# Performance work log

Measured on AMD Instinct MI355X. Metric: run time of the kernel, lower is better.

The kernel has to match this reference:

```python
import jax, jax.numpy as jnp
import numpy as np

EPS = 1e-8
NHEAD = 4
N_ITER = 3


def _ln(x, g, b):
    mu = jnp.mean(x, axis=-1, keepdims=True)
    var = jnp.var(x, axis=-1, keepdims=True)
    return (x - mu) / jnp.sqrt(var + 1e-5) * g + b


def _forward(inputs, eps, init_mu, init_logvar, Wk, Wv, Wq,
             ln_in_g, ln_in_b, ln_slot_g, ln_slot_b, ln_res_g, ln_res_b,
             gru_Wih, gru_Whh, gru_bih, gru_bhh, mlp_W1, mlp_W2, mlp_b2):
    B, N, _ = inputs.shape
    D = init_mu.shape[-1]
    dh = D // NHEAD
    # reparameterized init of the figure representation  [B, D]
    rep = init_mu + jnp.exp(0.5 * init_logvar) * eps
    x = _ln(inputs, ln_in_g, ln_in_b)
    # [B, H, N, dh]; k is pre-scaled by sqrt(nhead) as in the source
    k = (x @ Wk).reshape(B, N, NHEAD, dh).transpose(0, 2, 1, 3) * (NHEAD ** 0.5)
    v = (x @ Wv).reshape(B, N, NHEAD, dh).transpose(0, 2, 1, 3)

    def step(rep):
        q = (_ln(rep, ln_slot_g, ln_slot_b) @ Wq).reshape(B, NHEAD, dh)
        # sigmoid attention, normalized over the patch dim N
        w = jax.nn.sigmoid(jnp.einsum('bhnd,bhd->bhn', k, q)) + EPS
        w = w / jnp.sum(w, axis=2, keepdims=True)          # [B, H, N]
        att = jnp.einsum('bhn,bhnd->bhd', w, v).reshape(B, D)
        # GRUCell(input=att, hidden=rep)
        gi = att @ gru_Wih.T + gru_bih
        gh = rep @ gru_Whh.T + gru_bhh
        ir, iz, ig = jnp.split(gi, 3, axis=-1)
        hr, hz, hg = jnp.split(gh, 3, axis=-1)
        r = jax.nn.sigmoid(ir + hr)
        z = jax.nn.sigmoid(iz + hz)
        g = jnp.tanh(ig + r * hg)
        new = (1.0 - z) * g + z * rep
        # residual MLP
        new = new + jax.nn.relu(_ln(new, ln_res_g, ln_res_b) @ mlp_W1) @ mlp_W2 + mlp_b2
        return new, w

    for _ in range(N_ITER):
        rep, w = step(rep)
    # approx_implicit_grad: one extra step from a detached latent
    rep, w = step(jax.lax.stop_gradient(rep))
    return rep, jnp.sum(w, axis=1)[..., None]   # ([B, D], [B, N, 1])


def setup_inputs() -> dict:
    key = jax.random.key(0)
    ks = jax.random.split(key, 12)
    B, N, Din, D, H = 128, 4096, 256, 256, 1024
    s = lambda f: 1.0 / np.sqrt(f)
    return {
        'inputs': jax.random.normal(ks[0], (B, N, Din), jnp.float32),
        'eps': jax.random.normal(ks[1], (B, D), jnp.float32),
        'init_mu': jax.random.normal(ks[2], (1, D), jnp.float32) * 0.02,
        'init_logvar': jax.random.normal(ks[3], (1, D), jnp.float32) * 0.02,
        'Wk': jax.random.normal(ks[4], (Din, D), jnp.float32) * s(Din),
        'Wv': jax.random.normal(ks[5], (Din, D), jnp.float32) * s(Din),
        'Wq': jax.random.normal(ks[6], (D, D), jnp.float32) * s(D),
        'ln_in_g': jnp.ones((Din,), jnp.float32),
        'ln_in_b': jnp.zeros((Din,), jnp.float32),
        'ln_slot_g': jnp.ones((D,), jnp.float32),
        'ln_slot_b': jnp.zeros((D,), jnp.float32),
        'ln_res_g': jnp.ones((D,), jnp.float32),
        'ln_res_b': jnp.zeros((D,), jnp.float32),
        'gru_Wih': jax.random.normal(ks[7], (3 * D, D), jnp.float32) * s(D),
        'gru_Whh': jax.random.normal(ks[8], (3 * D, D), jnp.float32) * s(D),
        'gru_bih': jnp.zeros((3 * D,), jnp.float32),
        'gru_bhh': jnp.zeros((3 * D,), jnp.float32),
        'mlp_W1': jax.random.normal(ks[9], (D, H), jnp.float32) * s(D),
        'mlp_W2': jax.random.normal(ks[10], (H, D), jnp.float32) * s(H),
        'mlp_b2': jnp.zeros((D,), jnp.float32),
    }


def reference(inputs, eps, init_mu, init_logvar, Wk, Wv, Wq,
              ln_in_g, ln_in_b, ln_slot_g, ln_slot_b, ln_res_g, ln_res_b,
              gru_Wih, gru_Whh, gru_bih, gru_bhh, mlp_W1, mlp_W2, mlp_b2):
    return _forward(inputs, eps, init_mu, init_logvar, Wk, Wv, Wq,
                    ln_in_g, ln_in_b, ln_slot_g, ln_slot_b, ln_res_g, ln_res_b,
                    gru_Wih, gru_Whh, gru_bih, gru_bhh, mlp_W1, mlp_W2, mlp_b2)
```

## Files before the change

### kernel.cpp

```cpp
#include <hip/hip_runtime.h>
#include <hip/hip_bf16.h>

typedef __attribute__((ext_vector_type(2))) float f32x2;
typedef __attribute__((ext_vector_type(8))) unsigned short ushort8;
typedef __attribute__((ext_vector_type(4))) unsigned short ushort4_t;

#define N_    4096
#define NSPL1 2
#define NSPL2 2

__device__ inline float bf2f(unsigned short u){
  union{unsigned int i; float f;} c; c.i = ((unsigned int)u)<<16; return c.f;
}
__device__ inline unsigned short f2bf(float f){
  union{float f; unsigned int i;} c; c.f = f;
  unsigned int x = c.i;
  return (unsigned short)((x + 0x7fffu + ((x>>16)&1u)) >> 16);
}
__device__ inline float sigm(float s){ return 1.0f/(1.0f+__expf(-s)); }
__device__ inline f32x2 up2(unsigned int w){
  union{unsigned int i; float f;} lo, hi;
  lo.i = w<<16; hi.i = w & 0xffff0000u;
  f32x2 r; r.x = lo.f; r.y = hi.f; return r;
}

__device__ inline float rsum32(float v){
  union{float f; int i;} a, t;
  a.f = v;
  t.i = __builtin_amdgcn_update_dpp(0, a.i, 0x121, 0xF, 0xF, true); a.f += t.f;
  t.i = __builtin_amdgcn_update_dpp(0, a.i, 0x122, 0xF, 0xF, true); a.f += t.f;
  t.i = __builtin_amdgcn_update_dpp(0, a.i, 0x124, 0xF, 0xF, true); a.f += t.f;
  t.i = __builtin_amdgcn_update_dpp(0, a.i, 0x128, 0xF, 0xF, true); a.f += t.f;
  a.f += __shfl_xor(a.f, 16);
  return a.f;
}

__device__ inline float blkSum(float v, float* s4){
  v += __shfl_xor(v,1);  v += __shfl_xor(v,2);  v += __shfl_xor(v,4);
  v += __shfl_xor(v,8);  v += __shfl_xor(v,16); v += __shfl_xor(v,32);
  int lane = threadIdx.x & 63, w = threadIdx.x >> 6;
  __syncthreads();
  if (lane==0) s4[w] = v;
  __syncthreads();
  return s4[0]+s4[1]+s4[2]+s4[3];
}

__device__ inline float blkSum16(float v, float* s16){
  #pragma unroll
  for(int o=1;o<64;o<<=1) v += __shfl_xor(v,o);
  int lane = threadIdx.x & 63, w = threadIdx.x >> 6;
  __syncthreads();
  if (lane==0) s16[w] = v;
  __syncthreads();
  float r = 0.f;
  #pragma unroll
  for(int i=0;i<16;i++) r += s16[i];
  return r;
}

__global__ __launch_bounds__(256) void k_prep(
    const float* __restrict__ Wv, const float* __restrict__ Wih,
    const float* __restrict__ Whh, const float* __restrict__ W1,
    const float* __restrict__ W2, const float* __restrict__ Wq,
    const float* __restrict__ Wk,
    unsigned short* __restrict__ Wvp, unsigned short* __restrict__ Wip,
    unsigned short* __restrict__ Whp, unsigned short* __restrict__ W1p,
    unsigned short* __restrict__ W2p, unsigned short* __restrict__ Wqp,
    unsigned short* __restrict__ Wkp){
  int e = blockIdx.x*256 + threadIdx.x;
  if (e < 65536){
    int i = e&3, j = (e>>2)&255, pk = e>>10;
    Wvp[e] = f2bf(Wv[(4*pk+i)*256 + j]);
    Wqp[e] = f2bf(Wq[(4*pk+i)*256 + j]);
  }
  if (e < 196608){
    int i = e&3, j2 = e>>2;
    int j = j2 % 768, pk = j2 / 768;
    Wip[e] = f2bf(Wih[j*256 + 4*pk+i]);
    Whp[e] = f2bf(Whh[j*256 + 4*pk+i]);
  }
  {
    int i = e&3, j = (e>>2)&1023, pk = e>>12;
    W1p[e] = f2bf(W1[(4*pk+i)*1024 + j]);
  }
  {
    int i = e&3, j = (e>>2)&255, pk = e>>10;
    W2p[e] = f2bf(W2[(4*pk+i)*256 + j]);
  }
  if (e < 65536){
    int i = e&3, hc = (e>>2)&1023, pd = e>>12;
    int h = hc>>8, c = hc&255;
    Wkp[e] = f2bf(Wk[c*256 + h*64 + 4*pd+i]);
  }
}

__global__ __launch_bounds__(256) void k_init(
    const float* __restrict__ eps, const float* __restrict__ mu0,
    const float* __restrict__ lv0, const float* __restrict__ sg,
    const float* __restrict__ sb, const float* __restrict__ Wq,
    const unsigned short* __restrict__ Wkp,
    float* __restrict__ rep, float* __restrict__ p_out){
  __shared__ float s4[4]; __shared__ float xq[256]; __shared__ float q_s[256];
  int b = blockIdx.x, c = threadIdx.x;
  float r0 = mu0[c] + __expf(0.5f*lv0[c]) * eps[b*256+c];
  rep[b*256+c] = r0;
  float mu = blkSum(r0, s4) * (1.0f/256.0f);
  float df = r0 - mu;
  float var = blkSum(df*df, s4) * (1.0f/256.0f);
  float rs = rsqrtf(var + 1e-5f);
  xq[c] = df*rs*sg[c] + sb[c];
  __syncthreads();
  float a0=0,a1=0,a2=0,a3=0;
  for(int k=0;k<256;k+=4){
    a0 += xq[k  ]*Wq[(k  )*256+c];
    a1 += xq[k+1]*Wq[(k+1)*256+c];
    a2 += xq[k+2]*Wq[(k+2)*256+c];
    a3 += xq[k+3]*Wq[(k+3)*256+c];
  }
  q_s[c] = a0+a1+a2+a3;
  __syncthreads();
  #pragma unroll
  for(int h=0;h<4;h++){
    float acc = 0.f;
    for(int pd=0;pd<16;pd++){
      ushort4_t w4 = *reinterpret_cast<const ushort4_t*>(Wkp + ((size_t)pd*1024 + h*256 + c)*4);
      acc += bf2f(w4.x)*q_s[h*64+4*pd  ] + bf2f(w4.y)*q_s[h*64+4*pd+1]
           + bf2f(w4.z)*q_s[h*64+4*pd+2] + bf2f(w4.w)*q_s[h*64+4*pd+3];
    }
    p_out[b*1024 + h*256 + c] = 2.0f*acc;
  }
}

__global__ __launch_bounds__(1024) void k_lnattn(
    const float* __restrict__ in, const float* __restrict__ g,
    const float* __restrict__ bln, const float* __restrict__ p,
    unsigned short* __restrict__ x,
    float* __restrict__ u_part, float* __restrict__ ws_part){
  __shared__ float u_red[8][1024];
  __shared__ float ws_red[16][4];
  int split = blockIdx.x, b = blockIdx.y;
  int tid = threadIdx.x, wid = tid>>6, lane = tid&63;
  int grp = tid>>5, cl = tid&31;
  const int ROWS = N_ / NSPL1;
  const int NIT = ROWS/64;
  const float* pb = p + (size_t)b*1024;
  f32x2 pp2[4][4];
  #pragma unroll
  for(int h=0;h<4;h++){
    float4 pa = *reinterpret_cast<const float4*>(pb + h*256 + cl*8);
    float4 pc = *reinterpret_cast<const float4*>(pb + h*256 + cl*8 + 4);
    pp2[h][0] = f32x2{pa.x,pa.y}; pp2[h][1] = f32x2{pa.z,pa.w};
    pp2[h][2] = f32x2{pc.x,pc.y}; pp2[h][3] = f32x2{pc.z,pc.w};
  }
  float gg[8], bb[8];
  {
    float4 a = *reinterpret_cast<const float4*>(g + cl*8);
    float4 c = *reinterpret_cast<const float4*>(g + cl*8 + 4);
    gg[0]=a.x; gg[1]=a.y; gg[2]=a.z; gg[3]=a.w; gg[4]=c.x; gg[5]=c.y; gg[6]=c.z; gg[7]=c.w;
    a = *reinterpret_cast<const float4*>(bln + cl*8);
    c = *reinterpret_cast<const float4*>(bln + cl*8 + 4);
    bb[0]=a.x; bb[1]=a.y; bb[2]=a.z; bb[3]=a.w; bb[4]=c.x; bb[5]=c.y; bb[6]=c.z; bb[7]=c.w;
  }
  f32x2 u[4][4] = {};
  float wsum[4] = {0,0,0,0};
  const float* inb = in + ((size_t)b*N_ + split*ROWS)*256;
  unsigned short* xb = x + ((size_t)b*N_ + split*ROWS)*256;
  float4 a0 = *reinterpret_cast<const float4*>(inb + (size_t)grp*256 + cl*8);
  float4 c0 = *reinterpret_cast<const float4*>(inb + (size_t)grp*256 + cl*8 + 4);
  float4 a1 = *reinterpret_cast<const float4*>(inb + (size_t)(grp+32)*256 + cl*8);
  float4 c1 = *reinterpret_cast<const float4*>(inb + (size_t)(grp+32)*256 + cl*8 + 4);
  for(int it=0; it<NIT; ++it){
    int r0 = it*64 + grp, r1 = r0 + 32;
    float4 na, nc, nb1, nd1;
    if (it+1 < NIT){
      int p0 = (it+1)*64 + grp, p1 = p0 + 32;
      na  = *reinterpret_cast<const float4*>(inb + (size_t)p0*256 + cl*8);
      nc  = *reinterpret_cast<const float4*>(inb + (size_t)p0*256 + cl*8 + 4);
      nb1 = *reinterpret_cast<const float4*>(inb + (size_t)p1*256 + cl*8);
      nd1 = *reinterpret_cast<const float4*>(inb + (size_t)p1*256 + cl*8 + 4);
    }
    float sm0 = a0.x+a0.y+a0.z+a0.w + c0.x+c0.y+c0.z+c0.w;
    float sq0 = a0.x*a0.x+a0.y*a0.y+a0.z*a0.z+a0.w*a0.w
              + c0.x*c0.x+c0.y*c0.y+c0.z*c0.z+c0.w*c0.w;
    float sm1 = a1.x+a1.y+a1.z+a1.w + c1.x+c1.y+c1.z+c1.w;
    float sq1 = a1.x*a1.x+a1.y*a1.y+a1.z*a1.z+a1.w*a1.w
              + c1.x*c1.x+c1.y*c1.y+c1.z*c1.z+c1.w*c1.w;
    sm0 = rsum32(sm0); sq0 = rsum32(sq0);
    sm1 = rsum32(sm1); sq1 = rsum32(sq1);
    float mu0 = sm0*(1.0f/256.0f);
    float rs0 = rsqrtf(sq0*(1.0f/256.0f) - mu0*mu0 + 1e-5f);
    float mu1 = sm1*(1.0f/256.0f);
    float rs1 = rsqrtf(sq1*(1.0f/256.0f) - mu1*mu1 + 1e-5f);
    f32x2 px0[4], px1[4];
    px0[0].x=(a0.x-mu0)*rs0*gg[0]+bb[0]; px0[0].y=(a0.y-mu0)*rs0*gg[1]+bb[1];
    px0[1].x=(a0.z-mu0)*rs0*gg[2]+bb[2]; px0[1].y=(a0.w-mu0)*rs0*gg[3]+bb[3];
    px0[2].x=(c0.x-mu0)*rs0*gg[4]+bb[4]; px0[2].y=(c0.y-mu0)*rs0*gg[5]+bb[5];
    px0[3].x=(c0.z-mu0)*rs0*gg[6]+bb[6]; px0[3].y=(c0.w-mu0)*rs0*gg[7]+bb[7];
    px1[0].x=(a1.x-mu1)*rs1*gg[0]+bb[0]; px1[0].y=(a1.y-mu1)*rs1*gg[1]+bb[1];
    px1[1].x=(a1.z-mu1)*rs1*gg[2]+bb[2]; px1[1].y=(a1.w-mu1)*rs1*gg[3]+bb[3];
    px1[2].x=(c1.x-mu1)*rs1*gg[4]+bb[4]; px1[2].y=(c1.y-mu1)*rs1*gg[5]+bb[5];
    px1[3].x=(c1.z-mu1)*rs1*gg[6]+bb[6]; px1[3].y=(c1.w-mu1)*rs1*gg[7]+bb[7];
    ushort8 o8;
    o8[0]=f2bf(px0[0].x); o8[1]=f2bf(px0[0].y); o8[2]=f2bf(px0[1].x); o8[3]=f2bf(px0[1].y);
    o8[4]=f2bf(px0[2].x); o8[5]=f2bf(px0[2].y); o8[6]=f2bf(px0[3].x); o8[7]=f2bf(px0[3].y);
    *reinterpret_cast<ushort8*>(xb + (size_t)r0*256 + cl*8) = o8;
    o8[0]=f2bf(px1[0].x); o8[1]=f2bf(px1[0].y); o8[2]=f2bf(px1[1].x); o8[3]=f2bf(px1[1].y);
    o8[4]=f2bf(px1[2].x); o8[5]=f2bf(px1[2].y); o8[6]=f2bf(px1[3].x); o8[7]=f2bf(px1[3].y);
    *reinterpret_cast<ushort8*>(xb + (size_t)r1*256 + cl*8) = o8;
    float w0[4], w1[4];
    #pragma unroll
    for(int h=0;h<4;h++){
      f32x2 da = px0[0]*pp2[h][0] + px0[2]*pp2[h][2];
      f32x2 db = px0[1]*pp2[h][1] + px0[3]*pp2[h][3];
      da += db;
      float d0 = da.x + da.y;
      f32x2 ea = px1[0]*pp2[h][0] + px1[2]*pp2[h][2];
      f32x2 eb = px1[1]*pp2[h][1] + px1[3]*pp2[h][3];
      ea += eb;
      float d1 = ea.x + ea.y;
      d0 = rsum32(d0);
      d1 = rsum32(d1);
      w0[h] = sigm(d0) + 1e-8f;
      w1[h] = sigm(d1) + 1e-8f;
      wsum[h] += w0[h] + w1[h];
    }
    #pragma unroll
    for(int h=0;h<4;h++){
      f32x2 wa; wa.x = w0[h]; wa.y = w0[h];
      f32x2 wb; wb.x = w1[h]; wb.y = w1[h];
      #pragma unroll
      for(int j=0;j<4;j++){ u[h][j] += wa*px0[j]; u[h][j] += wb*px1[j]; }
    }
    a0 = na; c0 = nc; a1 = nb1; c1 = nd1;
  }
  #pragma unroll
  for(int h=0;h<4;h++){
    #pragma unroll
    for(int j=0;j<4;j++){
      u[h][j].x += __shfl_xor(u[h][j].x,32);
      u[h][j].y += __shfl_xor(u[h][j].y,32);
    }
    wsum[h] += __shfl_xor(wsum[h],32);
  }
  if (wid < 8 && lane < 32){
    #pragma unroll
    for(int h=0;h<4;h++){
      float4 a; a.x=u[h][0].x; a.y=u[h][0].y; a.z=u[h][1].x; a.w=u[h][1].y;
      float4 c; c.x=u[h][2].x; c.y=u[h][2].y; c.z=u[h][3].x; c.w=u[h][3].y;
      *reinterpret_cast<float4*>(&u_red[wid][h*256 + cl*8    ]) = a;
      *reinterpret_cast<float4*>(&u_red[wid][h*256 + cl*8 + 4]) = c;
    }
  }
  if (lane==0){
    #pragma unroll
    for(int h=0;h<4;h++) ws_red[wid][h] = wsum[h];
  }
  __syncthreads();
  if (wid >= 8 && lane < 32){
    #pragma unroll
    for(int h=0;h<4;h++){
      float4 a = *reinterpret_cast<const float4*>(&u_red[wid-8][h*256 + cl*8]);
      float4 c = *reinterpret_cast<const float4*>(&u_red[wid-8][h*256 + cl*8 + 4]);
      a.x+=u[h][0].x; a.y+=u[h][0].y; a.z+=u[h][1].x; a.w+=u[h][1].y;
      c.x+=u[h][2].x; c.y+=u[h][2].y; c.z+=u[h][3].x; c.w+=u[h][3].y;
      *reinterpret_cast<float4*>(&u_red[wid-8][h*256 + cl*8    ]) = a;
      *reinterpret_cast<float4*>(&u_red[wid-8][h*256 + cl*8 + 4]) = c;
    }
  }
  __syncthreads();
  {
    float s = 0.f;
    #pragma unroll
    for(int w=0;w<8;w++) s += u_red[w][tid];
    u_part[((size_t)split*128 + b)*1024 + tid] = s;
  }
  if (tid < 4){
    float s = 0.f;
    #pragma unroll
    for(int w=0;w<16;w++) s += ws_red[w][tid];
    ws_part[((size_t)split*128 + b)*4 + tid] = s;
  }
}

__global__ __launch_bounds__(1024) void k_attnstep(
    const unsigned short* __restrict__ x,
    const float* __restrict__ u_in, const float* __restrict__ ws_in,
    const float* __restrict__ rep_in, float* __restrict__ rep_out,
    const unsigned short* __restrict__ Wvp, const unsigned short* __restrict__ Wip,
    const unsigned short* __restrict__ Whp, const float* __restrict__ bih,
    const float* __restrict__ bhh, const float* __restrict__ ln_rg,
    const float* __restrict__ ln_rb, const unsigned short* __restrict__ W1p,
    const unsigned short* __restrict__ W2p, const float* __restrict__ b2,
    const float* __restrict__ ln_sg, const float* __restrict__ ln_sb,
    const unsigned short* __restrict__ Wqp, const unsigned short* __restrict__ Wkp,
    float* __restrict__ u_out, float* __restrict__ ws_out,
    float* __restrict__ w_buf, int write_w, int nsp_in){
  __shared__ float u_s[1024];
  __shared__ float att_s[256], rep_s[256], ln_s[256], nw_s[256], q_s[256];
  __shared__ float gi_s[768], gh_s[768];
  __shared__ float h1_s[1024], p_s[1024], red_a[1024];
  __shared__ float ws_s[4]; __shared__ float s16[16];
  __shared__ float u_red[8][1024];
  __shared__ float ws_red[16][4];
  int split = blockIdx.x, b = blockIdx.y;
  int tid = threadIdx.x;
  int c = tid & 255, s = tid >> 8;
  const int ROWS = N_ / NSPL2;
  const int NIT = ROWS/64;
  {
    float acc = 0.f;
    for(int sp=0; sp<nsp_in; ++sp)
      acc += u_in[((size_t)sp*128 + b)*1024 + tid];
    u_s[tid] = acc;
    if (tid < 4){
      float w = 0.f;
      for(int sp=0; sp<nsp_in; ++sp) w += ws_in[((size_t)sp*128 + b)*4 + tid];
      ws_s[tid] = w;
    }
    if (tid < 256) rep_s[tid] = rep_in[b*256 + tid];
  }
  __syncthreads();
  {
    const float* uh = u_s + (c>>6)*256;
    float a0 = 0.f, a1 = 0.f;
    for(int pk=s*16; pk<s*16+16; pk+=2){
      ushort4_t wa = *reinterpret_cast<const ushort4_t*>(Wvp + ((size_t)pk*256 + c)*4);
      ushort4_t wb = *reinterpret_cast<const ushort4_t*>(Wvp + ((size_t)(pk+1)*256 + c)*4);
      a0 += bf2f(wa.x)*uh[4*pk] + bf2f(wa.y)*uh[4*pk+1]
          + bf2f(wa.z)*uh[4*pk+2] + bf2f(wa.w)*uh[4*pk+3];
      a1 += bf2f(wb.x)*uh[4*pk+4] + bf2f(wb.y)*uh[4*pk+5]
          + bf2f(wb.z)*uh[4*pk+6] + bf2f(wb.w)*uh[4*pk+7];
    }
    red_a[tid] = a0+a1;
  }
  __syncthreads();
  if (tid < 256) att_s[tid] = (red_a[tid]+red_a[256+tid]+red_a[512+tid]+red_a[768+tid]) / ws_s[tid>>6];
  __syncthreads();
  if (tid < 768){
    float gi0=0.f, gi1=0.f, gh0=0.f, gh1=0.f;
    for(int pk=0;pk<64;pk+=2){
      ushort4_t wi0 = *reinterpret_cast<const ushort4_t*>(Wip + ((size_t)pk*768 + tid)*4);
      ushort4_t wh0 = *reinterpret_cast<const ushort4_t*>(Whp + ((size_t)pk*768 + tid)*4);
      ushort4_t wi1 = *reinterpret_cast<const ushort4_t*>(Wip + ((size_t)(pk+1)*768 + tid)*4);
      ushort4_t wh1 = *reinterpret_cast<const ushort4_t*>(Whp + ((size_t)(pk+1)*768 + tid)*4);
      gi0 += bf2f(wi0.x)*att_s[4*pk] + bf2f(wi0.y)*att_s[4*pk+1]
           + bf2f(wi0.z)*att_s[4*pk+2] + bf2f(wi0.w)*att_s[4*pk+3];
      gh0 += bf2f(wh0.x)*rep_s[4*pk] + bf2f(wh0.y)*rep_s[4*pk+1]
           + bf2f(wh0.z)*rep_s[4*pk+2] + bf2f(wh0.w)*rep_s[4*pk+3];
      gi1 += bf2f(wi1.x)*att_s[4*pk+4] + bf2f(wi1.y)*att_s[4*pk+5]
           + bf2f(wi1.z)*att_s[4*pk+6] + bf2f(wi1.w)*att_s[4*pk+7];
      gh1 += bf2f(wh1.x)*rep_s[4*pk+4] + bf2f(wh1.y)*rep_s[4*pk+5]
           + bf2f(wh1.z)*rep_s[4*pk+6] + bf2f(wh1.w)*rep_s[4*pk+7];
    }
    gi_s[tid] = gi0+gi1 + bih[tid];
    gh_s[tid] = gh0+gh1 + bhh[tid];
  }
  __syncthreads();
  if (tid < 256){
    float rr = sigm(gi_s[tid]     + gh_s[tid]);
    float zz = sigm(gi_s[256+tid] + gh_s[256+tid]);
    float t3 = tanhf(gi_s[512+tid] + rr*gh_s[512+tid]);
    nw_s[tid] = (1.f-zz)*t3 + zz*rep_s[tid];
  }
  __syncthreads();
  {
    float v = nw_s[c];
    float mu = blkSum16(v, s16)*(1.0f/1024.0f);
    float df = v - mu;
    float var = blkSum16(df*df, s16)*(1.0f/1024.0f);
    float rs = rsqrtf(var+1e-5f);
    if (s==0) ln_s[c] = df*rs*ln_rg[c]+ln_rb[c];
  }
  __syncthreads();
  {
    float a0 = 0.f, a1 = 0.f;
    for(int pk=0;pk<64;pk+=2){
      ushort4_t wa = *reinterpret_cast<const ushort4_t*>(W1p + ((size_t)pk*1024 + tid)*4);
      ushort4_t wb = *reinterpret_cast<const ushort4_t*>(W1p + ((size_t)(pk+1)*1024 + tid)*4);
      a0 += bf2f(wa.x)*ln_s[4*pk] + bf2f(wa.y)*ln_s[4*pk+1]
          + bf2f(wa.z)*ln_s[4*pk+2] + bf2f(wa.w)*ln_s[4*pk+3];
      a1 += bf2f(wb.x)*ln_s[4*pk+4] + bf2f(wb.y)*ln_s[4*pk+5]
          + bf2f(wb.z)*ln_s[4*pk+6] + bf2f(wb.w)*ln_s[4*pk+7];
    }
    h1_s[tid] = fmaxf(a0+a1, 0.f);
  }
  __syncthreads();
  {
    float a0 = 0.f, a1 = 0.f;
    for(int pk=s*64; pk<s*64+64; pk+=2){
      ushort4_t wa = *reinterpret_cast<const ushort4_t*>(W2p + ((size_t)pk*256 + c)*4);
      ushort4_t wb = *reinterpret_cast<const ushort4_t*>(W2p + ((size_t)(pk+1)*256 + c)*4);
      a0 += bf2f(wa.x)*h1_s[4*pk] + bf2f(wa.y)*h1_s[4*pk+1]
          + bf2f(wa.z)*h1_s[4*pk+2] + bf2f(wa.w)*h1_s[4*pk+3];
      a1 += bf2f(wb.x)*h1_s[4*pk+4] + bf2f(wb.y)*h1_s[4*pk+5]
          + bf2f(wb.z)*h1_s[4*pk+6] + bf2f(wb.w)*h1_s[4*pk+7];
    }
    red_a[tid] = a0+a1;
  }
  __syncthreads();
  if (tid < 256){
    float rn = nw_s[tid] + (red_a[tid]+red_a[256+tid]+red_a[512+tid]+red_a[768+tid]) + b2[tid];
    nw_s[tid] = rn;
    if (split==0) rep_out[b*256+tid] = rn;
  }
  __syncthreads();
  {
    float v = nw_s[c];
    float mu = blkSum16(v, s16)*(1.0f/1024.0f);
    float df = v - mu;
    float var = blkSum16(df*df, s16)*(1.0f/1024.0f);
    float rs = rsqrtf(var+1e-5f);
    if (s==0) ln_s[c] = df*rs*ln_sg[c]+ln_sb[c];
  }
  __syncthreads();
  {
    float a0 = 0.f, a1 = 0.f;
    for(int pk=s*16; pk<s*16+16; pk+=2){
      ushort4_t wa = *reinterpret_cast<const ushort4_t*>(Wqp + ((size_t)pk*256 + c)*4);
      ushort4_t wb = *reinterpret_cast<const ushort4_t*>(Wqp + ((size_t)(pk+1)*256 + c)*4);
      a0 += bf2f(wa.x)*ln_s[4*pk] + bf2f(wa.y)*ln_s[4*pk+1]
          + bf2f(wa.z)*ln_s[4*pk+2] + bf2f(wa.w)*ln_s[4*pk+3];
      a1 += bf2f(wb.x)*ln_s[4*pk+4] + bf2f(wb.y)*ln_s[4*pk+5]
          + bf2f(wb.z)*ln_s[4*pk+6] + bf2f(wb.w)*ln_s[4*pk+7];
    }
    red_a[tid] = a0+a1;
  }
  __syncthreads();
  if (tid < 256) q_s[tid] = red_a[tid]+red_a[256+tid]+red_a[512+tid]+red_a[768+tid];
  __syncthreads();
  {
    int h = tid>>8;
    float a0 = 0.f, a1 = 0.f;
    for(int pd=0;pd<16;pd+=2){
      ushort4_t wa = *reinterpret_cast<const ushort4_t*>(Wkp + ((size_t)pd*1024 + tid)*4);
      ushort4_t wb = *reinterpret_cast<const ushort4_t*>(Wkp + ((size_t)(pd+1)*1024 + tid)*4);
      a0 += bf2f(wa.x)*q_s[h*64+4*pd] + bf2f(wa.y)*q_s[h*64+4*pd+1]
          + bf2f(wa.z)*q_s[h*64+4*pd+2] + bf2f(wa.w)*q_s[h*64+4*pd+3];
      a1 += bf2f(wb.x)*q_s[h*64+4*pd+4] + bf2f(wb.y)*q_s[h*64+4*pd+5]
          + bf2f(wb.z)*q_s[h*64+4*pd+6] + bf2f(wb.w)*q_s[h*64+4*pd+7];
    }
    p_s[tid] = 2.0f*(a0+a1);
  }
  __syncthreads();
  int wid = tid>>6, lane = tid&63;
  int grp = tid>>5, cl = tid&31;
  f32x2 pp2[4][4];
  #pragma unroll
  for(int h=0;h<4;h++)
    #pragma unroll
    for(int j2=0;j2<4;j2++){
      pp2[h][j2].x = p_s[h*256 + cl*8 + j2*2];
      pp2[h][j2].y = p_s[h*256 + cl*8 + j2*2 + 1];
    }
  f32x2 u2[4][4] = {};
  float wsum[4] = {0,0,0,0};
  const unsigned short* xb = x + ((size_t)b*N_ + split*ROWS)*256;
  uint4 xa = *reinterpret_cast<const uint4*>(xb + (size_t)grp*256 + cl*8);
  uint4 xc = *reinterpret_cast<const uint4*>(xb + (size_t)(grp+32)*256 + cl*8);
  for(int it=0; it<NIT; ++it){
    int r0 = it*64 + grp, r1 = r0 + 32;
    uint4 nxa, nxc;
    if (it+1 < NIT){
      int p0 = (it+1)*64 + grp;
      nxa = *reinterpret_cast<const uint4*>(xb + (size_t)p0*256 + cl*8);
      nxc = *reinterpret_cast<const uint4*>(xb + (size_t)(p0+32)*256 + cl*8);
    }
    f32x2 x0[4], x1[4];
    x0[0]=up2(xa.x); x0[1]=up2(xa.y); x0[2]=up2(xa.z); x0[3]=up2(xa.w);
    x1[0]=up2(xc.x); x1[1]=up2(xc.y); x1[2]=up2(xc.z); x1[3]=up2(xc.w);
    float w0[4], w1[4];
    #pragma unroll
    for(int h=0;h<4;h++){
      f32x2 da = x0[0]*pp2[h][0] + x0[2]*pp2[h][2];
      f32x2 db = x0[1]*pp2[h][1] + x0[3]*pp2[h][3];
      da += db;
      float d0 = da.x + da.y;
      f32x2 ea = x1[0]*pp2[h][0] + x1[2]*pp2[h][2];
      f32x2 eb = x1[1]*pp2[h][1] + x1[3]*pp2[h][3];
      ea += eb;
      float d1 = ea.x + ea.y;
      d0 = rsum32(d0);
      d1 = rsum32(d1);
      w0[h] = sigm(d0) + 1e-8f;
      w1[h] = sigm(d1) + 1e-8f;
      wsum[h] += w0[h] + w1[h];
    }
    #pragma unroll
    for(int h=0;h<4;h++){
      f32x2 wa; wa.x = w0[h]; wa.y = w0[h];
      f32x2 wb; wb.x = w1[h]; wb.y = w1[h];
      #pragma unroll
      for(int j2=0;j2<4;j2++){ u2[h][j2] += wa*x0[j2]; u2[h][j2] += wb*x1[j2]; }
    }
    if (write_w && cl==0){
      float4 wv; wv.x=w0[0]; wv.y=w0[1]; wv.z=w0[2]; wv.w=w0[3];
      *reinterpret_cast<float4*>(w_buf + ((size_t)b*N_ + split*ROWS + r0)*4) = wv;
      float4 wz; wz.x=w1[0]; wz.y=w1[1]; wz.z=w1[2]; wz.w=w1[3];
      *reinterpret_cast<float4*>(w_buf + ((size_t)b*N_ + split*ROWS + r1)*4) = wz;
    }
    xa = nxa; xc = nxc;
  }
  #pragma unroll
  for(int h=0;h<4;h++){
    #pragma unroll
    for(int j2=0;j2<4;j2++){
      u2[h][j2].x += __shfl_xor(u2[h][j2].x,32);
      u2[h][j2].y += __shfl_xor(u2[h][j2].y,32);
    }
    wsum[h] += __shfl_xor(wsum[h],32);
  }
  __syncthreads();
  if (wid < 8 && lane < 32){
    #pragma unroll
    for(int h=0;h<4;h++){
      float4 a; a.x=u2[h][0].x; a.y=u2[h][0].y; a.z=u2[h][1].x; a.w=u2[h][1].y;
      float4 cc; cc.x=u2[h][2].x; cc.y=u2[h][2].y; cc.z=u2[h][3].x; cc.w=u2[h][3].y;
      *reinterpret_cast<float4*>(&u_red[wid][h*256 + cl*8    ]) = a;
      *reinterpret_cast<float4*>(&u_red[wid][h*256 + cl*8 + 4]) = cc;
    }
  }
  if (lane==0){
    #pragma unroll
    for(int h=0;h<4;h++) ws_red[wid][h] = wsum[h];
  }
  __syncthreads();
  if (wid >= 8 && lane < 32){
    #pragma unroll
    for(int h=0;h<4;h++){
      float4 a = *reinterpret_cast<const float4*>(&u_red[wid-8][h*256 + cl*8]);
      float4 cc = *reinterpret_cast<const float4*>(&u_red[wid-8][h*256 + cl*8 + 4]);
      a.x+=u2[h][0].x; a.y+=u2[h][0].y; a.z+=u2[h][1].x; a.w+=u2[h][1].y;
      cc.x+=u2[h][2].x; cc.y+=u2[h][2].y; cc.z+=u2[h][3].x; cc.w+=u2[h][3].y;
      *reinterpret_cast<float4*>(&u_red[wid-8][h*256 + cl*8    ]) = a;
      *reinterpret_cast<float4*>(&u_red[wid-8][h*256 + cl*8 + 4]) = cc;
    }
  }
  __syncthreads();
  {
    float sm = 0.f;
    #pragma unroll
    for(int w=0;w<8;w++) sm += u_red[w][tid];
    u_out[((size_t)split*128 + b)*1024 + tid] = sm;
  }
  if (tid < 4){
    float sm = 0.f;
    #pragma unroll
    for(int w=0;w<16;w++) sm += ws_red[w][tid];
    ws_out[((size_t)split*128 + b)*4 + tid] = sm;
  }
}

__global__ __launch_bounds__(1024) void k_finstep(
    const float* __restrict__ u_in, const float* __restrict__ ws_in,
    const float* __restrict__ rep_in,
    const unsigned short* __restrict__ Wvp, const unsigned short* __restrict__ Wip,
    const unsigned short* __restrict__ Whp, const float* __restrict__ bih,
    const float* __restrict__ bhh, const float* __restrict__ ln_rg,
    const float* __restrict__ ln_rb, const unsigned short* __restrict__ W1p,
    const unsigned short* __restrict__ W2p, const float* __restrict__ b2,
    float* __restrict__ out_rep, float* __restrict__ wsum_tot, int nsp_in){
  __shared__ float u_s[1024];
  __shared__ float att_s[256], rep_s[256], ln_s[256], nw_s[256];
  __shared__ float gi_s[768], gh_s[768];
  __shared__ float h1_s[1024], red_a[1024];
  __shared__ float ws_s[4]; __shared__ float s16[16];
  int b = blockIdx.x;
  int tid = threadIdx.x;
  int c = tid & 255, s = tid >> 8;
  {
    float acc = 0.f;
    for(int sp=0; sp<nsp_in; ++sp)
      acc += u_in[((size_t)sp*128 + b)*1024 + tid];
    u_s[tid] = acc;
    if (tid < 4){
      float w = 0.f;
      for(int sp=0; sp<nsp_in; ++sp) w += ws_in[((size_t)sp*128 + b)*4 + tid];
      ws_s[tid] = w; wsum_tot[b*4 + tid] = w;
    }
    if (tid < 256) rep_s[tid] = rep_in[b*256 + tid];
  }
  __syncthreads();
  {
    const float* uh = u_s + (c>>6)*256;
    float a0 = 0.f, a1 = 0.f;
    for(int pk=s*16; pk<s*16+16; pk+=2){
      ushort4_t wa = *reinterpret_cast<const ushort4_t*>(Wvp + ((size_t)pk*256 + c)*4);
      ushort4_t wb = *reinterpret_cast<const ushort4_t*>(Wvp + ((size_t)(pk+1)*256 + c)*4);
      a0 += bf2f(wa.x)*uh[4*pk] + bf2f(wa.y)*uh[4*pk+1]
          + bf2f(wa.z)*uh[4*pk+2] + bf2f(wa.w)*uh[4*pk+3];
      a1 += bf2f(wb.x)*uh[4*pk+4] + bf2f(wb.y)*uh[4*pk+5]
          + bf2f(wb.z)*uh[4*pk+6] + bf2f(wb.w)*uh[4*pk+7];
    }
    red_a[tid] = a0+a1;
  }
  __syncthreads();
  if (tid < 256) att_s[tid] = (red_a[tid]+red_a[256+tid]+red_a[512+tid]+red_a[768+tid]) / ws_s[tid>>6];
  __syncthreads();
  if (tid < 768){
    float gi0=0.f, gi1=0.f, gh0=0.f, gh1=0.f;
    for(int pk=0;pk<64;pk+=2){
      ushort4_t wi0 = *reinterpret_cast<const ushort4_t*>(Wip + ((size_t)pk*768 + tid)*4);
      ushort4_t wh0 = *reinterpret_cast<const ushort4_t*>(Whp + ((size_t)pk*768 + tid)*4);
      ushort4_t wi1 = *reinterpret_cast<const ushort4_t*>(Wip + ((size_t)(pk+1)*768 + tid)*4);
      ushort4_t wh1 = *reinterpret_cast<const ushort4_t*>(Whp + ((size_t)(pk+1)*768 + tid)*4);
      gi0 += bf2f(wi0.x)*att_s[4*pk] + bf2f(wi0.y)*att_s[4*pk+1]
           + bf2f(wi0.z)*att_s[4*pk+2] + bf2f(wi0.w)*att_s[4*pk+3];
      gh0 += bf2f(wh0.x)*rep_s[4*pk] + bf2f(wh0.y)*rep_s[4*pk+1]
           + bf2f(wh0.z)*rep_s[4*pk+2] + bf2f(wh0.w)*rep_s[4*pk+3];
      gi1 += bf2f(wi1.x)*att_s[4*pk+4] + bf2f(wi1.y)*att_s[4*pk+5]
           + bf2f(wi1.z)*att_s[4*pk+6] + bf2f(wi1.w)*att_s[4*pk+7];
      gh1 += bf2f(wh1.x)*rep_s[4*pk+4] + bf2f(wh1.y)*rep_s[4*pk+5]
           + bf2f(wh1.z)*rep_s[4*pk+6] + bf2f(wh1.w)*rep_s[4*pk+7];
    }
    gi_s[tid] = gi0+gi1 + bih[tid];
    gh_s[tid] = gh0+gh1 + bhh[tid];
  }
  __syncthreads();
  if (tid < 256){
    float rr = sigm(gi_s[tid]     + gh_s[tid]);
    float zz = sigm(gi_s[256+tid] + gh_s[256+tid]);
    float t3 = tanhf(gi_s[512+tid] + rr*gh_s[512+tid]);
    nw_s[tid] = (1.f-zz)*t3 + zz*rep_s[tid];
  }
  __syncthreads();
  {
    float v = nw_s[c];
    float mu = blkSum16(v, s16)*(1.0f/1024.0f);
    float df = v - mu;
    float var = blkSum16(df*df, s16)*(1.0f/1024.0f);
    float rs = rsqrtf(var+1e-5f);
    if (s==0) ln_s[c] = df*rs*ln_rg[c]+ln_rb[c];
  }
  __syncthreads();
  {
    float a0 = 0.f, a1 = 0.f;
    for(int pk=0;pk<64;pk+=2){
      ushort4_t wa = *reinterpret_cast<const ushort4_t*>(W1p + ((size_t)pk*1024 + tid)*4);
      ushort4_t wb = *reinterpret_cast<const ushort4_t*>(W1p + ((size_t)(pk+1)*1024 + tid)*4);
      a0 += bf2f(wa.x)*ln_s[4*pk] + bf2f(wa.y)*ln_s[4*pk+1]
          + bf2f(wa.z)*ln_s[4*pk+2] + bf2f(wa.w)*ln_s[4*pk+3];
      a1 += bf2f(wb.x)*ln_s[4*pk+4] + bf2f(wb.y)*ln_s[4*pk+5]
          + bf2f(wb.z)*ln_s[4*pk+6] + bf2f(wb.w)*ln_s[4*pk+7];
    }
    h1_s[tid] = fmaxf(a0+a1, 0.f);
  }
  __syncthreads();
  {
    float a0 = 0.f, a1 = 0.f;
    for(int pk=s*64; pk<s*64+64; pk+=2){
      ushort4_t wa = *reinterpret_cast<const ushort4_t*>(W2p + ((size_t)pk*256 + c)*4);
      ushort4_t wb = *reinterpret_cast<const ushort4_t*>(W2p + ((size_t)(pk+1)*256 + c)*4);
      a0 += bf2f(wa.x)*h1_s[4*pk] + bf2f(wa.y)*h1_s[4*pk+1]
          + bf2f(wa.z)*h1_s[4*pk+2] + bf2f(wa.w)*h1_s[4*pk+3];
      a1 += bf2f(wb.x)*h1_s[4*pk+4] + bf2f(wb.y)*h1_s[4*pk+5]
          + bf2f(wb.z)*h1_s[4*pk+6] + bf2f(wb.w)*h1_s[4*pk+7];
    }
    red_a[tid] = a0+a1;
  }
  __syncthreads();
  if (tid < 256){
    float rn = nw_s[tid] + (red_a[tid]+red_a[256+tid]+red_a[512+tid]+red_a[768+tid]) + b2[tid];
    out_rep[b*256+tid] = rn;
  }
}

__global__ __launch_bounds__(256) void k_wout(
    const float* __restrict__ w_buf, const float* __restrict__ wsum_tot,
    float* __restrict__ out){
  int idx = blockIdx.x*256 + threadIdx.x;
  int b = idx>>12;
  float4 w4 = *reinterpret_cast<const float4*>(w_buf + (size_t)idx*4);
  out[idx] = w4.x/wsum_tot[b*4+0] + w4.y/wsum_tot[b*4+1]
           + w4.z/wsum_tot[b*4+2] + w4.w/wsum_tot[b*4+3];
}

extern "C" void kernel_launch(void* const* d_in, const int* in_sizes, int n_in,
                              void* d_out, int out_size, void* d_ws, size_t ws_size,
                              hipStream_t stream){
  const float* inputs  = (const float*)d_in[0];
  const float* eps     = (const float*)d_in[1];
  const float* init_mu = (const float*)d_in[2];
  const float* init_lv = (const float*)d_in[3];
  const float* Wk      = (const float*)d_in[4];
  const float* Wv      = (const float*)d_in[5];
  const float* Wq      = (const float*)d_in[6];
  const float* ln_in_g = (const float*)d_in[7];
  const float* ln_in_b = (const float*)d_in[8];
  const float* ln_sg   = (const float*)d_in[9];
  const float* ln_sb   = (const float*)d_in[10];
  const float* ln_rg   = (const float*)d_in[11];
  const float* ln_rb   = (const float*)d_in[12];
  const float* Wih     = (const float*)d_in[13];
  const float* Whh     = (const float*)d_in[14];
  const float* bih     = (const float*)d_in[15];
  const float* bhh     = (const float*)d_in[16];
  const float* W1      = (const float*)d_in[17];
  const float* W2      = (const float*)d_in[18];
  const float* b2      = (const float*)d_in[19];

  char* ws = (char*)d_ws;
  size_t off = 0;
  auto alloc = [&](size_t bytes)->void*{
    void* p = ws + off; off += (bytes + 255) & ~(size_t)255; return p;
  };
  unsigned short* x   = (unsigned short*)alloc((size_t)128*N_*256*2);
  unsigned short* Wvp = (unsigned short*)alloc(65536*2);
  unsigned short* Wip = (unsigned short*)alloc(196608*2);
  unsigned short* Whp = (unsigned short*)alloc(196608*2);
  unsigned short* W1p = (unsigned short*)alloc(262144*2);
  unsigned short* W2p = (unsigned short*)alloc(262144*2);
  unsigned short* Wqp = (unsigned short*)alloc(65536*2);
  unsigned short* Wkp = (unsigned short*)alloc(65536*2);
  float* p0    = (float*)alloc((size_t)128*1024*4);
  float* uA    = (float*)alloc((size_t)NSPL1*128*1024*4);
  float* uB    = (float*)alloc((size_t)NSPL1*128*1024*4);
  float* wsA   = (float*)alloc(NSPL1*128*4*4);
  float* wsB   = (float*)alloc(NSPL1*128*4*4);
  float* repA  = (float*)alloc(128*256*4);
  float* repB  = (float*)alloc(128*256*4);
  float* wsum_tot = (float*)alloc(512*4);
  float* w_buf = (float*)alloc((size_t)128*N_*4*4);

  float* out_rep = (float*)d_out;
  float* out_w   = out_rep + 128*256;

  k_prep<<<1024,256,0,stream>>>(Wv,Wih,Whh,W1,W2,Wq,Wk, Wvp,Wip,Whp,W1p,W2p,Wqp,Wkp);
  k_init<<<128,256,0,stream>>>(eps, init_mu, init_lv, ln_sg, ln_sb, Wq, Wkp, repA, p0);
  k_lnattn<<<dim3(NSPL1,128),1024,0,stream>>>(inputs, ln_in_g, ln_in_b, p0, x, uA, wsA);
  k_attnstep<<<dim3(NSPL2,128),1024,0,stream>>>(x, uA, wsA, repA, repB,
      Wvp,Wip,Whp,bih,bhh,ln_rg,ln_rb,W1p,W2p,b2,ln_sg,ln_sb,Wqp,Wkp,
      uB, wsB, w_buf, 0, NSPL1);
  k_attnstep<<<dim3(NSPL2,128),1024,0,stream>>>(x, uB, wsB, repB, repA,
      Wvp,Wip,Whp,bih,bhh,ln_rg,ln_rb,W1p,W2p,b2,ln_sg,ln_sb,Wqp,Wkp,
      uA, wsA, w_buf, 0, NSPL2);
  k_attnstep<<<dim3(NSPL2,128),1024,0,stream>>>(x, uA, wsA, repA, repB,
      Wvp,Wip,Whp,bih,bhh,ln_rg,ln_rb,W1p,W2p,b2,ln_sg,ln_sb,Wqp,Wkp,
      uB, wsB, w_buf, 1, NSPL2);
  k_finstep<<<128,1024,0,stream>>>(uB, wsB, repB,
      Wvp,Wip,Whp,bih,bhh,ln_rg,ln_rb,W1p,W2p,b2, out_rep, wsum_tot, NSPL2);
  k_wout<<<2048,256,0,stream>>>(w_buf, wsum_tot, out_w);
}
```

Measured before the change: 547.0 us.

## Store normalized activations as FP8 with row-pair interleaved layout

The layer-normed input cache x changes from bf16 to fp8 (e4m3 via the hardware pack/convert builtins), with two consecutive rows interleaved per 32-bit word so one 16-byte load carries 8 columns of two rows. The first kernel writes this packed format, and the repeated attention-step kernel reads half the bytes per pass over x, unpacking directly into f32 pairs. This is meant to halve the dominant memory traffic of the repeated attention passes. It trades away accuracy, since fp8 has only 3 mantissa bits, and may push results past the tolerance.

```diff
diff --git a/kernel.cpp b/kernel.cpp
--- a/kernel.cpp
+++ b/kernel.cpp
@@ -18,10 +18,14 @@
   return (unsigned short)((x + 0x7fffu + ((x>>16)&1u)) >> 16);
 }
 __device__ inline float sigm(float s){ return 1.0f/(1.0f+__expf(-s)); }
-__device__ inline f32x2 up2(unsigned int w){
-  union{unsigned int i; float f;} lo, hi;
-  lo.i = w<<16; hi.i = w & 0xffff0000u;
-  f32x2 r; r.x = lo.f; r.y = hi.f; return r;
+
+template<bool HI>
+__device__ inline f32x2 up8(unsigned int w){
+  return __builtin_amdgcn_cvt_pk_f32_fp8((int)w, HI);
+}
+template<bool HI>
+__device__ inline unsigned int pk8(float a, float b, unsigned int old){
+  return (unsigned int)__builtin_amdgcn_cvt_pk_fp8_f32(a, b, (int)old, HI);
 }
 
 __device__ inline float rsum32(float v){
@@ -134,7 +138,7 @@
 __global__ __launch_bounds__(1024) void k_lnattn(
     const float* __restrict__ in, const float* __restrict__ g,
     const float* __restrict__ bln, const float* __restrict__ p,
-    unsigned short* __restrict__ x,
+    unsigned char* __restrict__ x,
     float* __restrict__ u_part, float* __restrict__ ws_part){
   __shared__ float u_red[8][1024];
   __shared__ float ws_red[16][4];
@@ -164,20 +168,20 @@
   f32x2 u[4][4] = {};
   float wsum[4] = {0,0,0,0};
   const float* inb = in + ((size_t)b*N_ + split*ROWS)*256;
-  unsigned short* xb = x + ((size_t)b*N_ + split*ROWS)*256;
-  float4 a0 = *reinterpret_cast<const float4*>(inb + (size_t)grp*256 + cl*8);
-  float4 c0 = *reinterpret_cast<const float4*>(inb + (size_t)grp*256 + cl*8 + 4);
-  float4 a1 = *reinterpret_cast<const float4*>(inb + (size_t)(grp+32)*256 + cl*8);
-  float4 c1 = *reinterpret_cast<const float4*>(inb + (size_t)(grp+32)*256 + cl*8 + 4);
+  unsigned char* xb = x + ((size_t)b*N_ + split*ROWS)*256;
+  float4 a0 = *reinterpret_cast<const float4*>(inb + (size_t)(2*grp)*256 + cl*8);
+  float4 c0 = *reinterpret_cast<const float4*>(inb + (size_t)(2*grp)*256 + cl*8 + 4);
+  float4 a1 = *reinterpret_cast<const float4*>(inb + (size_t)(2*grp+1)*256 + cl*8);
+  float4 c1 = *reinterpret_cast<const float4*>(inb + (size_t)(2*grp+1)*256 + cl*8 + 4);
   for(int it=0; it<NIT; ++it){
-    int r0 = it*64 + grp, r1 = r0 + 32;
+    int r0 = it*64 + 2*grp;
     float4 na, nc, nb1, nd1;
     if (it+1 < NIT){
-      int p0 = (it+1)*64 + grp, p1 = p0 + 32;
+      int p0 = (it+1)*64 + 2*grp;
       na  = *reinterpret_cast<const float4*>(inb + (size_t)p0*256 + cl*8);
       nc  = *reinterpret_cast<const float4*>(inb + (size_t)p0*256 + cl*8 + 4);
-      nb1 = *reinterpret_cast<const float4*>(inb + (size_t)p1*256 + cl*8);
-      nd1 = *reinterpret_cast<const float4*>(inb + (size_t)p1*256 + cl*8 + 4);
+      nb1 = *reinterpret_cast<const float4*>(inb + (size_t)(p0+1)*256 + cl*8);
+      nd1 = *reinterpret_cast<const float4*>(inb + (size_t)(p0+1)*256 + cl*8 + 4);
     }
     float sm0 = a0.x+a0.y+a0.z+a0.w + c0.x+c0.y+c0.z+c0.w;
     float sq0 = a0.x*a0.x+a0.y*a0.y+a0.z*a0.z+a0.w*a0.w
@@ -200,13 +204,17 @@
     px1[1].x=(a1.z-mu1)*rs1*gg[2]+bb[2]; px1[1].y=(a1.w-mu1)*rs1*gg[3]+bb[3];
     px1[2].x=(c1.x-mu1)*rs1*gg[4]+bb[4]; px1[2].y=(c1.y-mu1)*rs1*gg[5]+bb[5];
     px1[3].x=(c1.z-mu1)*rs1*gg[6]+bb[6]; px1[3].y=(c1.w-mu1)*rs1*gg[7]+bb[7];
-    ushort8 o8;
-    o8[0]=f2bf(px0[0].x); o8[1]=f2bf(px0[0].y); o8[2]=f2bf(px0[1].x); o8[3]=f2bf(px0[1].y);
-    o8[4]=f2bf(px0[2].x); o8[5]=f2bf(px0[2].y); o8[6]=f2bf(px0[3].x); o8[7]=f2bf(px0[3].y);
-    *reinterpret_cast<ushort8*>(xb + (size_t)r0*256 + cl*8) = o8;
-    o8[0]=f2bf(px1[0].x); o8[1]=f2bf(px1[0].y); o8[2]=f2bf(px1[1].x); o8[3]=f2bf(px1[1].y);
-    o8[4]=f2bf(px1[2].x); o8[5]=f2bf(px1[2].y); o8[6]=f2bf(px1[3].x); o8[7]=f2bf(px1[3].y);
-    *reinterpret_cast<ushort8*>(xb + (size_t)r1*256 + cl*8) = o8;
+    uint4 st;
+    unsigned int pk_;
+    pk_  = pk8<false>(px0[0].x, px1[0].x, 0u);
+    st.x = pk8<true >(px0[0].y, px1[0].y, pk_);
+    pk_  = pk8<false>(px0[1].x, px1[1].x, 0u);
+    st.y = pk8<true >(px0[1].y, px1[1].y, pk_);
+    pk_  = pk8<false>(px0[2].x, px1[2].x, 0u);
+    st.z = pk8<true >(px0[2].y, px1[2].y, pk_);
+    pk_  = pk8<false>(px0[3].x, px1[3].x, 0u);
+    st.w = pk8<true >(px0[3].y, px1[3].y, pk_);
+    *reinterpret_cast<uint4*>(xb + (size_t)(r0>>1)*512 + cl*16) = st;
     float w0[4], w1[4];
     #pragma unroll
     for(int h=0;h<4;h++){
@@ -283,7 +291,7 @@
 }
 
 __global__ __launch_bounds__(1024) void k_attnstep(
-    const unsigned short* __restrict__ x,
+    const unsigned char* __restrict__ x,
     const float* __restrict__ u_in, const float* __restrict__ ws_in,
     const float* __restrict__ rep_in, float* __restrict__ rep_out,
     const unsigned short* __restrict__ Wvp, const unsigned short* __restrict__ Wip,
@@ -444,77 +452,76 @@
   __syncthreads();
   int wid = tid>>6, lane = tid&63;
   int grp = tid>>5, cl = tid&31;
-  f32x2 pp2[4][4];
+  float pp[4][8];
   #pragma unroll
   for(int h=0;h<4;h++)
     #pragma unroll
-    for(int j2=0;j2<4;j2++){
-      pp2[h][j2].x = p_s[h*256 + cl*8 + j2*2];
-      pp2[h][j2].y = p_s[h*256 + cl*8 + j2*2 + 1];
-    }
-  f32x2 u2[4][4] = {};
+    for(int j=0;j<8;j++) pp[h][j] = p_s[h*256 + cl*8 + j];
+  f32x2 uacc2[4][8] = {};
   float wsum[4] = {0,0,0,0};
-  const unsigned short* xb = x + ((size_t)b*N_ + split*ROWS)*256;
-  uint4 xa = *reinterpret_cast<const uint4*>(xb + (size_t)grp*256 + cl*8);
-  uint4 xc = *reinterpret_cast<const uint4*>(xb + (size_t)(grp+32)*256 + cl*8);
+  const unsigned char* xb = x + ((size_t)b*N_ + split*ROWS)*256;
+  uint4 xa = *reinterpret_cast<const uint4*>(xb + (size_t)grp*512 + cl*16);
   for(int it=0; it<NIT; ++it){
-    int r0 = it*64 + grp, r1 = r0 + 32;
-    uint4 nxa, nxc;
+    int pi = it*32 + grp;
+    uint4 nxa;
     if (it+1 < NIT){
-      int p0 = (it+1)*64 + grp;
-      nxa = *reinterpret_cast<const uint4*>(xb + (size_t)p0*256 + cl*8);
-      nxc = *reinterpret_cast<const uint4*>(xb + (size_t)(p0+32)*256 + cl*8);
-    }
-    f32x2 x0[4], x1[4];
-    x0[0]=up2(xa.x); x0[1]=up2(xa.y); x0[2]=up2(xa.z); x0[3]=up2(xa.w);
-    x1[0]=up2(xc.x); x1[1]=up2(xc.y); x1[2]=up2(xc.z); x1[3]=up2(xc.w);
+      int qi = (it+1)*32 + grp;
+      nxa = *reinterpret_cast<const uint4*>(xb + (size_t)qi*512 + cl*16);
+    }
+    f32x2 t[8];
+    t[0]=up8<false>(xa.x); t[1]=up8<true>(xa.x);
+    t[2]=up8<false>(xa.y); t[3]=up8<true>(xa.y);
+    t[4]=up8<false>(xa.z); t[5]=up8<true>(xa.z);
+    t[6]=up8<false>(xa.w); t[7]=up8<true>(xa.w);
     float w0[4], w1[4];
     #pragma unroll
     for(int h=0;h<4;h++){
-      f32x2 da = x0[0]*pp2[h][0] + x0[2]*pp2[h][2];
-      f32x2 db = x0[1]*pp2[h][1] + x0[3]*pp2[h][3];
-      da += db;
-      float d0 = da.x + da.y;
-      f32x2 ea = x1[0]*pp2[h][0] + x1[2]*pp2[h][2];
-      f32x2 eb = x1[1]*pp2[h][1] + x1[3]*pp2[h][3];
-      ea += eb;
-      float d1 = ea.x + ea.y;
-      d0 = rsum32(d0);
-      d1 = rsum32(d1);
+      f32x2 acc0 = t[0]*pp[h][0];
+      f32x2 acc1 = t[1]*pp[h][1];
+      acc0 += t[2]*pp[h][2];
+      acc1 += t[3]*pp[h][3];
+      acc0 += t[4]*pp[h][4];
+      acc1 += t[5]*pp[h][5];
+      acc0 += t[6]*pp[h][6];
+      acc1 += t[7]*pp[h][7];
+      acc0 += acc1;
+      float d0 = rsum32(acc0.x);
+      float d1 = rsum32(acc0.y);
       w0[h] = sigm(d0) + 1e-8f;
       w1[h] = sigm(d1) + 1e-8f;
       wsum[h] += w0[h] + w1[h];
     }
     #pragma unroll
     for(int h=0;h<4;h++){
-      f32x2 wa; wa.x = w0[h]; wa.y = w0[h];
-      f32x2 wb; wb.x = w1[h]; wb.y = w1[h];
+      f32x2 wv; wv.x = w0[h]; wv.y = w1[h];
       #pragma unroll
-      for(int j2=0;j2<4;j2++){ u2[h][j2] += wa*x0[j2]; u2[h][j2] += wb*x1[j2]; }
+      for(int j=0;j<8;j++) uacc2[h][j] += wv*t[j];
     }
     if (write_w && cl==0){
       float4 wv; wv.x=w0[0]; wv.y=w0[1]; wv.z=w0[2]; wv.w=w0[3];
-      *reinterpret_cast<float4*>(w_buf + ((size_t)b*N_ + split*ROWS + r0)*4) = wv;
+      *reinterpret_cast<float4*>(w_buf + ((size_t)b*N_ + split*ROWS + 2*pi)*4) = wv;
       float4 wz; wz.x=w1[0]; wz.y=w1[1]; wz.z=w1[2]; wz.w=w1[3];
-      *reinterpret_cast<float4*>(w_buf + ((size_t)b*N_ + split*ROWS + r1)*4) = wz;
-    }
-    xa = nxa; xc = nxc;
-  }
+      *reinterpret_cast<float4*>(w_buf + ((size_t)b*N_ + split*ROWS + 2*pi+1)*4) = wz;
+    }
+    xa = nxa;
+  }
+  float uf[4][8];
   #pragma unroll
-  for(int h=0;h<4;h++){
-    #pragma unroll
-    for(int j2=0;j2<4;j2++){
-      u2[h][j2].x += __shfl_xor(u2[h][j2].x,32);
-      u2[h][j2].y += __shfl_xor(u2[h][j2].y,32);
-    }
-    wsum[h] += __shfl_xor(wsum[h],32);
-  }
+  for(int h=0;h<4;h++)
+    #pragma unroll
+    for(int j=0;j<8;j++){
+      float v = uacc2[h][j].x + uacc2[h][j].y;
+      v += __shfl_xor(v,32);
+      uf[h][j] = v;
+    }
+  #pragma unroll
+  for(int h=0;h<4;h++) wsum[h] += __shfl_xor(wsum[h],32);
   __syncthreads();
   if (wid < 8 && lane < 32){
     #pragma unroll
     for(int h=0;h<4;h++){
-      float4 a; a.x=u2[h][0].x; a.y=u2[h][0].y; a.z=u2[h][1].x; a.w=u2[h][1].y;
-      float4 cc; cc.x=u2[h][2].x; cc.y=u2[h][2].y; cc.z=u2[h][3].x; cc.w=u2[h][3].y;
+      float4 a; a.x=uf[h][0]; a.y=uf[h][1]; a.z=uf[h][2]; a.w=uf[h][3];
+      float4 cc; cc.x=uf[h][4]; cc.y=uf[h][5]; cc.z=uf[h][6]; cc.w=uf[h][7];
       *reinterpret_cast<float4*>(&u_red[wid][h*256 + cl*8    ]) = a;
       *reinterpret_cast<float4*>(&u_red[wid][h*256 + cl*8 + 4]) = cc;
     }
@@ -529,8 +536,8 @@
     for(int h=0;h<4;h++){
       float4 a = *reinterpret_cast<const float4*>(&u_red[wid-8][h*256 + cl*8]);
       float4 cc = *reinterpret_cast<const float4*>(&u_red[wid-8][h*256 + cl*8 + 4]);
-      a.x+=u2[h][0].x; a.y+=u2[h][0].y; a.z+=u2[h][1].x; a.w+=u2[h][1].y;
-      cc.x+=u2[h][2].x; cc.y+=u2[h][2].y; cc.z+=u2[h][3].x; cc.w+=u2[h][3].y;
+      a.x+=uf[h][0]; a.y+=uf[h][1]; a.z+=uf[h][2]; a.w+=uf[h][3];
+      cc.x+=uf[h][4]; cc.y+=uf[h][5]; cc.z+=uf[h][6]; cc.w+=uf[h][7];
       *reinterpret_cast<float4*>(&u_red[wid-8][h*256 + cl*8    ]) = a;
       *reinterpret_cast<float4*>(&u_red[wid-8][h*256 + cl*8 + 4]) = cc;
     }
@@ -703,7 +710,7 @@
   auto alloc = [&](size_t bytes)->void*{
     void* p = ws + off; off += (bytes + 255) & ~(size_t)255; return p;
   };
-  unsigned short* x   = (unsigned short*)alloc((size_t)128*N_*256*2);
+  unsigned char* x    = (unsigned char*)alloc((size_t)128*N_*256);
   unsigned short* Wvp = (unsigned short*)alloc(65536*2);
   unsigned short* Wip = (unsigned short*)alloc(196608*2);
   unsigned short* Whp = (unsigned short*)alloc(196608*2);
```

After: 1.126 ms. 106% more time.
